# Optimization experiments

Measured on AMD Instinct MI355X. Metric: run time of the kernel, lower is better.

The kernel has to match this reference:

```python
import jax, jax.numpy as jnp
import numpy as np

B, S, E, H = 4, 2048, 1024, 16
D = E // H  # head_dim = 64

def setup_inputs() -> dict:
    key = jax.random.key(0)
    k1, k2, k3 = jax.random.split(key, 3)
    x = jax.random.normal(k1, (B, S, E), dtype=jnp.float32)
    # Linear weights stored as [in, out] so y = x @ W (torch Linear uses W^T; same math).
    w_att = jax.random.normal(k2, (E, 3 * E), dtype=jnp.float32) * (1.0 / np.sqrt(E))
    w_proj = jax.random.normal(k3, (E, E), dtype=jnp.float32) * (1.0 / np.sqrt(E))
    return {"x": x, "w_att": w_att, "w_proj": w_proj}

def reference(x, w_att, w_proj):
    b, s, e = x.shape
    qkv = x @ w_att                      # [b, s, 3e]
    q, k, v = jnp.split(qkv, 3, axis=-1)
    # [b, h, s, d]
    q = q.reshape(b, s, H, D).transpose(0, 2, 1, 3)
    k = k.reshape(b, s, H, D).transpose(0, 2, 1, 3)
    v = v.reshape(b, s, H, D).transpose(0, 2, 1, 3)
    scale = 1.0 / np.sqrt(D)
    att = jnp.einsum('bhqd,bhkd->bhqk', q, k) * scale  # [b, h, s, s]
    causal = jnp.tril(jnp.ones((s, s), dtype=bool))
    att = jnp.where(causal[None, None], att, jnp.finfo(att.dtype).min)
    att = jax.nn.softmax(att, axis=-1)
    y = jnp.einsum('bhqk,bhkd->bhqd', att, v)          # [b, h, s, d]
    y = y.transpose(0, 2, 1, 3).reshape(b, s, e)
    return y @ w_proj
```

## Files before the change

### kernel.cpp

```cpp
#include <hip/hip_runtime.h>
#include <hip/hip_bf16.h>

typedef __bf16 b16v8 __attribute__((ext_vector_type(8)));
typedef __bf16 b16v4 __attribute__((ext_vector_type(4)));
typedef float  f32x4 __attribute__((ext_vector_type(4)));

#define BB 4
#define SS 2048
#define EE 1024
#define HH 16
#define DD 64

#define QSCALE 0.18033688011112042f
#define CMAX 20.0f

__device__ __forceinline__ void async16(const __bf16* g, __bf16* l) {
  typedef __attribute__((address_space(1))) const unsigned int gu32;
  typedef __attribute__((address_space(3))) unsigned int lu32;
  __builtin_amdgcn_global_load_lds((gu32*)g, (lu32*)l, 16, 0, 0);
}

__device__ __forceinline__ f32x4 mfma16x16x16_bf16(b16v4 a, b16v4 b, f32x4 c) {
#if __has_builtin(__builtin_amdgcn_mfma_f32_16x16x16_bf16)
  return __builtin_amdgcn_mfma_f32_16x16x16_bf16(a, b, c, 0, 0, 0);
#else
  typedef short s16v4 __attribute__((ext_vector_type(4)));
  union U { b16v4 h; s16v4 s; };
  U ua, ub; ua.h = a; ub.h = b;
  return __builtin_amdgcn_mfma_f32_16x16x16bf16_1k(ua.s, ub.s, c, 0, 0, 0);
#endif
}

__global__ __launch_bounds__(256) void prep_kernel(const float* __restrict__ x,
                                                   __bf16* __restrict__ xb,
                                                   const float* __restrict__ w_att,
                                                   __bf16* __restrict__ watt,
                                                   const float* __restrict__ w_proj,
                                                   __bf16* __restrict__ wproj) {
  __shared__ float t[32][33];
  const int bid = blockIdx.x;
  if (bid < 8192) {
    int i = bid * 256 + threadIdx.x;
    float4 f = ((const float4*)x)[i];
    b16v4 o = {(__bf16)f.x, (__bf16)f.y, (__bf16)f.z, (__bf16)f.w};
    ((b16v4*)xb)[i] = o;
    return;
  }
  const float* w;
  __bf16* wt;
  int N, local;
  if (bid < 11264) { w = w_att; wt = watt; N = 3072; local = bid - 8192; }
  else             { w = w_proj; wt = wproj; N = 1024; local = bid - 11264; }
  const int K = 1024;
  int n0 = (local % (N >> 5)) * 32, k0 = (local / (N >> 5)) * 32;
  int tx = threadIdx.x & 31, ty = threadIdx.x >> 5;
#pragma unroll
  for (int j = 0; j < 32; j += 8)
    t[ty + j][tx] = w[(size_t)(k0 + ty + j) * N + n0 + tx];
  __syncthreads();
#pragma unroll
  for (int j = 0; j < 32; j += 8)
    wt[(size_t)(n0 + ty + j) * K + k0 + tx] = (__bf16)t[tx][ty + j];
}

__global__ __launch_bounds__(256) void gemm_qkv(const __bf16* __restrict__ A,
                                                const __bf16* __restrict__ Bt,
                                                __bf16* __restrict__ qb,
                                                __bf16* __restrict__ kb,
                                                __bf16* __restrict__ vtb,
                                                int K) {
  __shared__ __bf16 a_lds[2][256 * 32];
  __shared__ __bf16 b_lds[2][128 * 32];
  const int tid = threadIdx.x;
  const int lane = tid & 63;
  const int w = tid >> 6;
  const int wm = (w >> 1) * 128, wn = (w & 1) * 64;
  const int l16 = lane & 15, quad = lane >> 4;

  const int gx = gridDim.x;
  const int nwg = gx * gridDim.y;
  const int bid0 = blockIdx.y * gx + blockIdx.x;
  const int qq = nwg >> 3;
  const int xcd = bid0 & 7, idx = bid0 >> 3;
  const int wgid = xcd * qq + idx;
  const int bxx = wgid % gx, byy = wgid / gx;

  const __bf16* Ab = A + (size_t)byy * 256 * K;
  const __bf16* Bb = Bt + (size_t)bxx * 128 * K;

  auto stage = [&](int k0, int bufi) {
#pragma unroll
    for (int i = 0; i < 4; ++i) {
      int c = tid + i * 256;
      int row = c >> 2, ch = c & 3;
      async16(Ab + (size_t)row * K + k0 + ((ch ^ (row & 3)) * 8), a_lds[bufi] + c * 8);
    }
#pragma unroll
    for (int i = 0; i < 2; ++i) {
      int c = tid + i * 256;
      int row = c >> 2, ch = c & 3;
      async16(Bb + (size_t)row * K + k0 + ((ch ^ (row & 3)) * 8), b_lds[bufi] + c * 8);
    }
  };

  f32x4 acc[8][4];
#pragma unroll
  for (int i = 0; i < 8; ++i)
#pragma unroll
    for (int j = 0; j < 4; ++j) acc[i][j] = f32x4{0.f, 0.f, 0.f, 0.f};

  stage(0, 0);
  const int KT = K >> 5;
  const int sw = (quad ^ (l16 & 3)) * 8;
  for (int kt = 0; kt < KT; ++kt) {
    __syncthreads();
    if (kt + 1 < KT) stage((kt + 1) << 5, (kt + 1) & 1);
    const __bf16* ab = a_lds[kt & 1];
    const __bf16* bb = b_lds[kt & 1];
    b16v8 af[8], bf4[4];
#pragma unroll
    for (int t = 0; t < 8; ++t)
      af[t] = *(const b16v8*)(ab + (wm + t * 16 + l16) * 32 + sw);
#pragma unroll
    for (int t = 0; t < 4; ++t)
      bf4[t] = *(const b16v8*)(bb + (wn + t * 16 + l16) * 32 + sw);
#pragma unroll
    for (int mt = 0; mt < 8; ++mt)
#pragma unroll
      for (int nt = 0; nt < 4; ++nt)
        acc[mt][nt] = __builtin_amdgcn_mfma_f32_16x16x32_bf16(af[mt], bf4[nt], acc[mt][nt], 0, 0, 0);
  }

#pragma unroll
  for (int mt = 0; mt < 8; ++mt)
#pragma unroll
    for (int nt = 0; nt < 4; ++nt) {
      int row = byy * 256 + wm + mt * 16 + quad * 4;
      int col = bxx * 128 + wn + nt * 16 + l16;
      int b = row >> 11, s = row & 2047;
      int sec = col >> 10, cc = col & 1023;
      int h = cc >> 6, d = cc & 63;
      if (sec == 2) {
        b16v4 vv = {(__bf16)acc[mt][nt][0], (__bf16)acc[mt][nt][1],
                    (__bf16)acc[mt][nt][2], (__bf16)acc[mt][nt][3]};
        *(b16v4*)(vtb + ((size_t)(b * HH + h) * DD + d) * SS + s) = vv;
      } else {
        __bf16* dst = (sec == 0) ? qb : kb;
        float sc = (sec == 0) ? QSCALE : 1.0f;
#pragma unroll
        for (int r = 0; r < 4; ++r)
          dst[(((size_t)(b * HH + h) * SS + s + r) << 6) + d] = (__bf16)(acc[mt][nt][r] * sc);
      }
    }
}

__global__ __launch_bounds__(256) void gemm_proj(const __bf16* __restrict__ A,
                                                 const __bf16* __restrict__ Bt,
                                                 float* __restrict__ out,
                                                 int N, int K) {
  __shared__ __bf16 a_lds[2][128 * 32];
  __shared__ __bf16 b_lds[2][64 * 32];
  const int tid = threadIdx.x;
  const int lane = tid & 63;
  const int w = tid >> 6;
  const int wm = (w >> 1) * 64, wn = (w & 1) * 32;
  const int l16 = lane & 15, quad = lane >> 4;

  const int gx = gridDim.x;
  const int nwg = gx * gridDim.y;
  const int bid0 = blockIdx.y * gx + blockIdx.x;
  const int qq = nwg >> 3;
  const int xcd = bid0 & 7, idx = bid0 >> 3;
  const int wgid = xcd * qq + idx;
  const int bxx = wgid % gx, byy = wgid / gx;

  const __bf16* Ab = A + (size_t)byy * 128 * K;
  const __bf16* Bb = Bt + (size_t)bxx * 64 * K;

  auto stage = [&](int k0, int bufi) {
#pragma unroll
    for (int i = 0; i < 2; ++i) {
      int c = tid + i * 256;
      int row = c >> 2, ch = c & 3;
      async16(Ab + (size_t)row * K + k0 + ((ch ^ (row & 3)) * 8), a_lds[bufi] + c * 8);
    }
    {
      int c = tid;
      int row = c >> 2, ch = c & 3;
      async16(Bb + (size_t)row * K + k0 + ((ch ^ (row & 3)) * 8), b_lds[bufi] + c * 8);
    }
  };

  f32x4 acc[4][2];
#pragma unroll
  for (int i = 0; i < 4; ++i)
#pragma unroll
    for (int j = 0; j < 2; ++j) acc[i][j] = f32x4{0.f, 0.f, 0.f, 0.f};

  stage(0, 0);
  const int KT = K >> 5;
  const int sw = (quad ^ (l16 & 3)) * 8;
  for (int kt = 0; kt < KT; ++kt) {
    __syncthreads();
    if (kt + 1 < KT) stage((kt + 1) << 5, (kt + 1) & 1);
    const __bf16* ab = a_lds[kt & 1];
    const __bf16* bb = b_lds[kt & 1];
    b16v8 af[4], bf4[2];
#pragma unroll
    for (int t = 0; t < 4; ++t)
      af[t] = *(const b16v8*)(ab + (wm + t * 16 + l16) * 32 + sw);
#pragma unroll
    for (int t = 0; t < 2; ++t)
      bf4[t] = *(const b16v8*)(bb + (wn + t * 16 + l16) * 32 + sw);
#pragma unroll
    for (int mt = 0; mt < 4; ++mt)
#pragma unroll
      for (int nt = 0; nt < 2; ++nt)
        acc[mt][nt] = __builtin_amdgcn_mfma_f32_16x16x32_bf16(af[mt], bf4[nt], acc[mt][nt], 0, 0, 0);
  }

#pragma unroll
  for (int mt = 0; mt < 4; ++mt)
#pragma unroll
    for (int nt = 0; nt < 2; ++nt)
#pragma unroll
      for (int r = 0; r < 4; ++r) {
        int row = byy * 128 + wm + mt * 16 + quad * 4 + r;
        int col = bxx * 64 + wn + nt * 16 + l16;
        out[(size_t)row * N + col] = acc[mt][nt][r];
      }
}

__global__ __launch_bounds__(256, 4) void attn_kernel(const __bf16* __restrict__ qb,
                                                      const __bf16* __restrict__ kb,
                                                      const __bf16* __restrict__ vtb,
                                                      __bf16* __restrict__ y) {
  __shared__ __bf16 kv_lds[2][8192];
  const int tid = threadIdx.x;
  const int lane = tid & 63;
  const int w = tid >> 6;
  const int l16 = lane & 15, quad = lane >> 4;
  const int bh = blockIdx.x, p = blockIdx.y;
  const int b = bh >> 4, h = bh & 15;
  const __bf16* kbase = kb + (size_t)bh * SS * DD;
  const __bf16* vtbase = vtb + (size_t)bh * DD * SS;

  const int e = l16 & 7;
  const int koff0 = l16 * 64 + ((quad ^ e) * 8);
  const int koff1 = l16 * 64 + (((quad + 4) ^ e) * 8);
  int voff[4];
#pragma unroll
  for (int kf = 0; kf < 4; ++kf)
    voff[kf] = 4096 + l16 * 64 + (((kf * 2 + (quad >> 1)) ^ e) * 8) + ((quad & 1) * 4);

  int gK[2], gV[2], lK[2], lV[2];
#pragma unroll
  for (int i = 0; i < 2; ++i) {
    int L = tid + i * 256;
    int row = L >> 3, c = L & 7;
    gK[i] = row * DD + ((c ^ (row & 7)) * 8);
    lK[i] = L * 8;
    gV[i] = row * SS + ((c ^ (row & 7)) * 8);
    lV[i] = 4096 + L * 8;
  }
  auto stage = [&](int j, __bf16* buf) {
    const __bf16* kj = kbase + j * (64 * DD);
    const __bf16* vj = vtbase + j * 64;
#pragma unroll
    for (int i = 0; i < 2; ++i) async16(kj + gK[i], buf + lK[i]);
#pragma unroll
    for (int i = 0; i < 2; ++i) async16(vj + gV[i], buf + lV[i]);
  };

#pragma unroll
  for (int t = 0; t < 2; ++t) {
    const int qt = (t == 0) ? (31 - p) : p;

    b16v8 qf[2];
#pragma unroll
    for (int ks = 0; ks < 2; ++ks)
      qf[ks] = *(const b16v8*)(qb + ((size_t)bh * SS + qt * 64 + w * 16 + l16) * DD + ks * 32 + quad * 8);

    f32x4 o[4];
#pragma unroll
    for (int dt = 0; dt < 4; ++dt) o[dt] = f32x4{0.f, 0.f, 0.f, 0.f};
    f32x4 lv = {0.f, 0.f, 0.f, 0.f};

    __syncthreads();
    stage(0, kv_lds[0]);

    for (int j = 0; j <= qt; ++j) {
      __syncthreads();
      if (j < qt) stage(j + 1, kv_lds[(j + 1) & 1]);
      const __bf16* buf = kv_lds[0] + ((j & 1) << 13);

      f32x4 s[4];
#pragma unroll
      for (int kf = 0; kf < 4; ++kf) s[kf] = f32x4{-CMAX, -CMAX, -CMAX, -CMAX};
      __builtin_amdgcn_s_setprio(1);
#pragma unroll
      for (int kf = 0; kf < 4; ++kf) {
        b16v8 k0 = *(const b16v8*)(buf + koff0 + kf * 1024);
        b16v8 k1 = *(const b16v8*)(buf + koff1 + kf * 1024);
        s[kf] = __builtin_amdgcn_mfma_f32_16x16x32_bf16(k0, qf[0], s[kf], 0, 0, 0);
        s[kf] = __builtin_amdgcn_mfma_f32_16x16x32_bf16(k1, qf[1], s[kf], 0, 0, 0);
      }
      __builtin_amdgcn_s_setprio(0);
      if (j == qt) {
        int ql = w * 16 + l16;
#pragma unroll
        for (int kf = 0; kf < 4; ++kf)
#pragma unroll
          for (int r = 0; r < 4; ++r)
            if (kf * 16 + quad * 4 + r > ql) s[kf][r] = -1e30f;
      }
#pragma unroll
      for (int kf = 0; kf < 4; ++kf)
#pragma unroll
        for (int r = 0; r < 4; ++r) s[kf][r] = __builtin_amdgcn_exp2f(s[kf][r]);
      lv += (s[0] + s[1]) + (s[2] + s[3]);
      __builtin_amdgcn_s_setprio(1);
#pragma unroll
      for (int kf = 0; kf < 4; ++kf) {
        b16v4 pf = {(__bf16)s[kf][0], (__bf16)s[kf][1], (__bf16)s[kf][2], (__bf16)s[kf][3]};
#pragma unroll
        for (int dt = 0; dt < 4; ++dt) {
          b16v4 vf = *(const b16v4*)(buf + voff[kf] + dt * 1024);
          o[dt] = mfma16x16x16_bf16(vf, pf, o[dt]);
        }
      }
      __builtin_amdgcn_s_setprio(0);
    }

    float lr = (lv[0] + lv[1]) + (lv[2] + lv[3]);
    lr += __shfl_xor(lr, 16);
    lr += __shfl_xor(lr, 32);
    float inv = 1.0f / lr;
    int q = qt * 64 + w * 16 + l16;
#pragma unroll
    for (int dt = 0; dt < 4; ++dt) {
      b16v4 ov = {(__bf16)(o[dt][0] * inv), (__bf16)(o[dt][1] * inv),
                  (__bf16)(o[dt][2] * inv), (__bf16)(o[dt][3] * inv)};
      *(b16v4*)(y + ((size_t)b * SS + q) * EE + h * 64 + dt * 16 + quad * 4) = ov;
    }
  }
}

extern "C" void kernel_launch(void* const* d_in, const int* in_sizes, int n_in,
                              void* d_out, int out_size, void* d_ws, size_t ws_size,
                              hipStream_t stream) {
  (void)in_sizes; (void)n_in; (void)out_size; (void)ws_size;
  const float* x = (const float*)d_in[0];
  const float* w_att = (const float*)d_in[1];
  const float* w_proj = (const float*)d_in[2];
  float* out = (float*)d_out;

  char* ws = (char*)d_ws;
  size_t off = 0;
  auto alloc = [&](size_t elems) { __bf16* p = (__bf16*)(ws + off); off += elems * 2; return p; };
  __bf16* xb = alloc(8388608);
  __bf16* qb = alloc(8388608);
  __bf16* kb = alloc(8388608);
  __bf16* vtb = alloc(8388608);
  __bf16* watt = alloc(3145728);
  __bf16* wproj = alloc(1048576);

  prep_kernel<<<12288, 256, 0, stream>>>(x, xb, w_att, watt, w_proj, wproj);
  gemm_qkv<<<dim3(24, 32), 256, 0, stream>>>(xb, watt, qb, kb, vtb, 1024);
  attn_kernel<<<dim3(64, 16), 256, 0, stream>>>(qb, kb, vtb, xb);
  gemm_proj<<<dim3(16, 64), 256, 0, stream>>>(xb, wproj, out, 1024, 1024);
}
```

Baseline: 274.4 us.

## Triple-buffer GEMM LDS with vmcnt waits and halve QKV tile height

Both GEMM kernels move from a double-buffered LDS pipeline with __syncthreads to a three-stage ring. Each iteration prefetches two k-tiles ahead and waits with explicit s_waitcnt vmcnt counts plus a raw s_barrier, so global loads overlap longer with MFMA work. The QKV GEMM tile also shrinks from 256x128 to 128x128, doubling the grid to 1536 workgroups and halving accumulator registers for better occupancy. The risks are lower per-tile reuse and correctness that depends on the hand-counted vmcnt values matching the number of issued async loads.

```diff
diff --git a/kernel.cpp b/kernel.cpp
--- a/kernel.cpp
+++ b/kernel.cpp
@@ -69,12 +69,12 @@
                                                 __bf16* __restrict__ kb,
                                                 __bf16* __restrict__ vtb,
                                                 int K) {
-  __shared__ __bf16 a_lds[2][256 * 32];
-  __shared__ __bf16 b_lds[2][128 * 32];
+  __shared__ __bf16 a_lds[3][128 * 32];
+  __shared__ __bf16 b_lds[3][128 * 32];
   const int tid = threadIdx.x;
   const int lane = tid & 63;
   const int w = tid >> 6;
-  const int wm = (w >> 1) * 128, wn = (w & 1) * 64;
+  const int wm = (w >> 1) * 64, wn = (w & 1) * 64;
   const int l16 = lane & 15, quad = lane >> 4;
 
   const int gx = gridDim.x;
@@ -85,12 +85,12 @@
   const int wgid = xcd * qq + idx;
   const int bxx = wgid % gx, byy = wgid / gx;
 
-  const __bf16* Ab = A + (size_t)byy * 256 * K;
+  const __bf16* Ab = A + (size_t)byy * 128 * K;
   const __bf16* Bb = Bt + (size_t)bxx * 128 * K;
 
   auto stage = [&](int k0, int bufi) {
 #pragma unroll
-    for (int i = 0; i < 4; ++i) {
+    for (int i = 0; i < 2; ++i) {
       int c = tid + i * 256;
       int row = c >> 2, ch = c & 3;
       async16(Ab + (size_t)row * K + k0 + ((ch ^ (row & 3)) * 8), a_lds[bufi] + c * 8);
@@ -103,39 +103,46 @@
     }
   };
 
-  f32x4 acc[8][4];
-#pragma unroll
-  for (int i = 0; i < 8; ++i)
+  f32x4 acc[4][4];
+#pragma unroll
+  for (int i = 0; i < 4; ++i)
 #pragma unroll
     for (int j = 0; j < 4; ++j) acc[i][j] = f32x4{0.f, 0.f, 0.f, 0.f};
 
   stage(0, 0);
+  stage(32, 1);
   const int KT = K >> 5;
   const int sw = (quad ^ (l16 & 3)) * 8;
+  int cur = 0;
   for (int kt = 0; kt < KT; ++kt) {
-    __syncthreads();
-    if (kt + 1 < KT) stage((kt + 1) << 5, (kt + 1) & 1);
-    const __bf16* ab = a_lds[kt & 1];
-    const __bf16* bb = b_lds[kt & 1];
-    b16v8 af[8], bf4[4];
-#pragma unroll
-    for (int t = 0; t < 8; ++t)
+    if (kt + 1 < KT) asm volatile("s_waitcnt vmcnt(4)" ::: "memory");
+    else             asm volatile("s_waitcnt vmcnt(0)" ::: "memory");
+    __builtin_amdgcn_s_barrier();
+    if (kt + 2 < KT) {
+      int stb = cur + 2; if (stb > 2) stb -= 3;
+      stage((kt + 2) << 5, stb);
+    }
+    const __bf16* ab = a_lds[cur];
+    const __bf16* bb = b_lds[cur];
+    b16v8 af[4], bf4[4];
+#pragma unroll
+    for (int t = 0; t < 4; ++t) {
       af[t] = *(const b16v8*)(ab + (wm + t * 16 + l16) * 32 + sw);
-#pragma unroll
-    for (int t = 0; t < 4; ++t)
       bf4[t] = *(const b16v8*)(bb + (wn + t * 16 + l16) * 32 + sw);
-#pragma unroll
-    for (int mt = 0; mt < 8; ++mt)
+    }
+#pragma unroll
+    for (int mt = 0; mt < 4; ++mt)
 #pragma unroll
       for (int nt = 0; nt < 4; ++nt)
         acc[mt][nt] = __builtin_amdgcn_mfma_f32_16x16x32_bf16(af[mt], bf4[nt], acc[mt][nt], 0, 0, 0);
-  }
-
-#pragma unroll
-  for (int mt = 0; mt < 8; ++mt)
+    cur = (cur == 2) ? 0 : cur + 1;
+  }
+
+#pragma unroll
+  for (int mt = 0; mt < 4; ++mt)
 #pragma unroll
     for (int nt = 0; nt < 4; ++nt) {
-      int row = byy * 256 + wm + mt * 16 + quad * 4;
+      int row = byy * 128 + wm + mt * 16 + quad * 4;
       int col = bxx * 128 + wn + nt * 16 + l16;
       int b = row >> 11, s = row & 2047;
       int sec = col >> 10, cc = col & 1023;
@@ -158,8 +165,8 @@
                                                  const __bf16* __restrict__ Bt,
                                                  float* __restrict__ out,
                                                  int N, int K) {
-  __shared__ __bf16 a_lds[2][128 * 32];
-  __shared__ __bf16 b_lds[2][64 * 32];
+  __shared__ __bf16 a_lds[3][128 * 32];
+  __shared__ __bf16 b_lds[3][64 * 32];
   const int tid = threadIdx.x;
   const int lane = tid & 63;
   const int w = tid >> 6;
@@ -198,13 +205,20 @@
     for (int j = 0; j < 2; ++j) acc[i][j] = f32x4{0.f, 0.f, 0.f, 0.f};
 
   stage(0, 0);
+  stage(32, 1);
   const int KT = K >> 5;
   const int sw = (quad ^ (l16 & 3)) * 8;
+  int cur = 0;
   for (int kt = 0; kt < KT; ++kt) {
-    __syncthreads();
-    if (kt + 1 < KT) stage((kt + 1) << 5, (kt + 1) & 1);
-    const __bf16* ab = a_lds[kt & 1];
-    const __bf16* bb = b_lds[kt & 1];
+    if (kt + 1 < KT) asm volatile("s_waitcnt vmcnt(3)" ::: "memory");
+    else             asm volatile("s_waitcnt vmcnt(0)" ::: "memory");
+    __builtin_amdgcn_s_barrier();
+    if (kt + 2 < KT) {
+      int stb = cur + 2; if (stb > 2) stb -= 3;
+      stage((kt + 2) << 5, stb);
+    }
+    const __bf16* ab = a_lds[cur];
+    const __bf16* bb = b_lds[cur];
     b16v8 af[4], bf4[2];
 #pragma unroll
     for (int t = 0; t < 4; ++t)
@@ -217,6 +231,7 @@
 #pragma unroll
       for (int nt = 0; nt < 2; ++nt)
         acc[mt][nt] = __builtin_amdgcn_mfma_f32_16x16x32_bf16(af[mt], bf4[nt], acc[mt][nt], 0, 0, 0);
+    cur = (cur == 2) ? 0 : cur + 1;
   }
 
 #pragma unroll
@@ -366,7 +381,7 @@
   __bf16* wproj = alloc(1048576);
 
   prep_kernel<<<12288, 256, 0, stream>>>(x, xb, w_att, watt, w_proj, wproj);
-  gemm_qkv<<<dim3(24, 32), 256, 0, stream>>>(xb, watt, qb, kb, vtb, 1024);
+  gemm_qkv<<<dim3(24, 64), 256, 0, stream>>>(xb, watt, qb, kb, vtb, 1024);
   attn_kernel<<<dim3(64, 16), 256, 0, stream>>>(qb, kb, vtb, xb);
   gemm_proj<<<dim3(16, 64), 256, 0, stream>>>(xb, wproj, out, 1024, 1024);
 }
```

Result: faster. 235.8 us, median of 2 (-14.1%).
